# Kernel optimization log

Hardware: AMD Instinct MI355X
Metric: run time of the kernel (lower is better)

Reference implementation:

```python
import jax, jax.numpy as jnp
import numpy as np

C = 2000
P = 5_000_000
FX, FY, CX, CY = 1000.0, 1000.0, 320.0, 240.0


def setup_inputs() -> dict:
    key = jax.random.key(0)
    k1, k2, k3, k4, k5 = jax.random.split(key, 5)
    # SE3 poses: [tx,ty,tz, qx,qy,qz,qw] with unit quaternion (pypose randn_SE3 convention)
    t = jax.random.normal(k1, (C, 3), dtype=jnp.float32)
    q = jax.random.normal(k2, (C, 4), dtype=jnp.float32)
    q = q / jnp.linalg.norm(q, axis=-1, keepdims=True)
    poses = jnp.concatenate([t, q], axis=-1)  # [C,7]
    points_param = jax.random.normal(k3, (P, 3), dtype=jnp.float32)
    observes = jax.random.normal(k4, (P, 2), dtype=jnp.float32)
    K = jnp.array([[FX, 0.0, CX], [0.0, FY, CY], [0.0, 0.0, 1.0]], dtype=jnp.float32)
    cidx = jax.random.randint(k5, (P,), 0, C, dtype=jnp.int64)
    pidx = jnp.arange(P, dtype=jnp.int64)
    return {"poses": poses, "points_param": points_param, "observes": observes,
            "K": K, "cidx": cidx, "pidx": pidx}


def _se3_act(pose7, pts):
    # pose7: [P,7] = [t(3), q_xyz(3), q_w(1)]; pts: [P,3]
    t = pose7[:, 0:3]
    qv = pose7[:, 3:6]
    qw = pose7[:, 6:7]
    # rotated = p + 2*qv x (qv x p + qw*p)
    uv = jnp.cross(qv, pts) + qw * pts
    return pts + 2.0 * jnp.cross(qv, uv) + t


def reference(poses, points_param, observes, K, cidx, pidx):
    p = poses[cidx]            # [P,7] gather camera poses
    pts = points_param[pidx]   # [P,3] gather 3D points
    pc = _se3_act(p, pts)      # camera-frame points [P,3]
    proj = pc @ K.T            # [P,3] homogeneous pixels
    pix = proj[:, :2] / proj[:, 2:3]
    return pix - observes      # [P,2] residual
```

## Files before the change

### kernel.cpp

```cpp
#include <hip/hip_runtime.h>


__global__ __launch_bounds__(256) void residual_kernel(
    const float* __restrict__ poses,
    const float* __restrict__ pts,
    const float* __restrict__ obs,
    const float* __restrict__ Km,
    const int*   __restrict__ cidx,
    const int*   __restrict__ pidx,
    float*       __restrict__ out,
    int n4)
{
    int t = blockIdx.x * blockDim.x + threadIdx.x;
    if (t >= n4) return;

    float k00 = Km[0], k01 = Km[1], k02 = Km[2];
    float k10 = Km[3], k11 = Km[4], k12 = Km[5];
    float k20 = Km[6], k21 = Km[7], k22 = Km[8];

    int4 ci4 = ((const int4*)cidx)[t];
    int4 pi4 = ((const int4*)pidx)[t];
    float4 ob01 = ((const float4*)obs)[2 * t];
    float4 ob23 = ((const float4*)obs)[2 * t + 1];

    int cis[4]  = {ci4.x, ci4.y, ci4.z, ci4.w};
    int pis[4]  = {pi4.x, pi4.y, pi4.z, pi4.w};
    float ob[8] = {ob01.x, ob01.y, ob01.z, ob01.w, ob23.x, ob23.y, ob23.z, ob23.w};

    float res[8];

    #pragma unroll
    for (int j = 0; j < 4; ++j) {
        const float* pp = pts + 3L * (long)pis[j];
        float px = pp[0], py = pp[1], pz = pp[2];

        const float* po = poses + 7L * (long)cis[j];
        float tx = po[0], ty = po[1], tz = po[2];
        float qx = po[3], qy = po[4], qz = po[5], qw = po[6];

        float ux = qy * pz - qz * py + qw * px;
        float uy = qz * px - qx * pz + qw * py;
        float uz = qx * py - qy * px + qw * pz;

        float cx = px + 2.0f * (qy * uz - qz * uy) + tx;
        float cy = py + 2.0f * (qz * ux - qx * uz) + ty;
        float cz = pz + 2.0f * (qx * uy - qy * ux) + tz;

        float w    = k20 * cx + k21 * cy + k22 * cz;
        float invw = 1.0f / w;
        float u    = (k00 * cx + k01 * cy + k02 * cz) * invw;
        float v    = (k10 * cx + k11 * cy + k12 * cz) * invw;

        res[2 * j]     = u - ob[2 * j];
        res[2 * j + 1] = v - ob[2 * j + 1];
    }

    float4* o = (float4*)(out + 8L * (long)t);
    o[0] = make_float4(res[0], res[1], res[2], res[3]);
    o[1] = make_float4(res[4], res[5], res[6], res[7]);
}

extern "C" void kernel_launch(void* const* d_in, const int* in_sizes, int n_in,
                              void* d_out, int out_size, void* d_ws, size_t ws_size,
                              hipStream_t stream) {
    const float* poses = (const float*)d_in[0];
    const float* pts   = (const float*)d_in[1];
    const float* obs   = (const float*)d_in[2];
    const float* Km    = (const float*)d_in[3];
    const int*   cidx  = (const int*)d_in[4];
    const int*   pidx  = (const int*)d_in[5];
    float* out = (float*)d_out;

    int P  = in_sizes[4];
    int n4 = P / 4;

    const int block = 256;
    int grid = (n4 + block - 1) / block;
    residual_kernel<<<grid, block, 0, stream>>>(poses, pts, obs, Km, cidx, pidx, out, n4);
}
```

Baseline: 197.9 us.

## Stage camera poses in LDS and switch to persistent grid-stride kernel

Each block copies all C poses into shared memory, packed as two float4 slots per camera with a parity swizzle, and then serves per-observation pose reads from LDS instead of scattered global loads. The launch becomes a fixed 512x1024 persistent grid with a grid-stride loop so the staging cost is paid once per block. In exchange, every block performs a serial preload of 64KB of LDS data with strided global reads, and the large LDS footprint limits occupancy. The pose table was small and probably already L2-resident, so the benefit depends on how much the global gathers were actually costing.

Result: slower. 202.5 us (+2.3%).

```diff
diff --git a/kernel.cpp b/kernel.cpp
--- a/kernel.cpp
+++ b/kernel.cpp
@@ -1,7 +1,10 @@
 #include <hip/hip_runtime.h>
 
 
-__global__ __launch_bounds__(256) void residual_kernel(
+#define BLOCK 1024
+#define GRID  512
+
+__global__ __launch_bounds__(BLOCK) void residual_kernel(
     const float* __restrict__ poses,
     const float* __restrict__ pts,
     const float* __restrict__ obs,
@@ -9,55 +12,76 @@
     const int*   __restrict__ cidx,
     const int*   __restrict__ pidx,
     float*       __restrict__ out,
-    int n4)
+    int n4,
+    int C)
 {
-    int t = blockIdx.x * blockDim.x + threadIdx.x;
-    if (t >= n4) return;
+    extern __shared__ float spose[];
+
+    int tid = threadIdx.x;
+    int total = C * 7;
+    for (int idx = tid; idx < total; idx += BLOCK) {
+        int j = idx / 7;
+        int k = idx - j * 7;
+        int par  = j & 1;
+        int slot = (k < 4) ? (2 * j + par) : (2 * j + 1 - par);
+        int off  = (k < 4) ? k : (k - 4);
+        spose[slot * 4 + off] = poses[idx];
+    }
+    __syncthreads();
+
+    const float4* sp = (const float4*)spose;
 
     float k00 = Km[0], k01 = Km[1], k02 = Km[2];
     float k10 = Km[3], k11 = Km[4], k12 = Km[5];
     float k20 = Km[6], k21 = Km[7], k22 = Km[8];
 
-    int4 ci4 = ((const int4*)cidx)[t];
-    int4 pi4 = ((const int4*)pidx)[t];
-    float4 ob01 = ((const float4*)obs)[2 * t];
-    float4 ob23 = ((const float4*)obs)[2 * t + 1];
+    int stride = GRID * BLOCK;
+    for (int t = blockIdx.x * BLOCK + tid; t < n4; t += stride) {
+        int4 ci4 = ((const int4*)cidx)[t];
+        int4 pi4 = ((const int4*)pidx)[t];
+        float4 ob01 = ((const float4*)obs)[2 * t];
+        float4 ob23 = ((const float4*)obs)[2 * t + 1];
 
-    int cis[4]  = {ci4.x, ci4.y, ci4.z, ci4.w};
-    int pis[4]  = {pi4.x, pi4.y, pi4.z, pi4.w};
-    float ob[8] = {ob01.x, ob01.y, ob01.z, ob01.w, ob23.x, ob23.y, ob23.z, ob23.w};
+        int cis[4]  = {ci4.x, ci4.y, ci4.z, ci4.w};
+        int pis[4]  = {pi4.x, pi4.y, pi4.z, pi4.w};
+        float ob[8] = {ob01.x, ob01.y, ob01.z, ob01.w,
+                       ob23.x, ob23.y, ob23.z, ob23.w};
 
-    float res[8];
+        float res[8];
 
-    #pragma unroll
-    for (int j = 0; j < 4; ++j) {
-        const float* pp = pts + 3L * (long)pis[j];
-        float px = pp[0], py = pp[1], pz = pp[2];
+        #pragma unroll
+        for (int j = 0; j < 4; ++j) {
+            const float* pp = pts + 3L * (long)pis[j];
+            float px = pp[0], py = pp[1], pz = pp[2];
 
-        const float* po = poses + 7L * (long)cis[j];
-        float tx = po[0], ty = po[1], tz = po[2];
-        float qx = po[3], qy = po[4], qz = po[5], qw = po[6];
+            int ci  = cis[j];
+            int par = ci & 1;
+            float4 lo = sp[2 * ci + par];
+            float4 hi = sp[2 * ci + 1 - par];
+            float tx = lo.x, ty = lo.y, tz = lo.z;
+            float qx = lo.w, qy = hi.x, qz = hi.y, qw = hi.z;
 
-        float ux = qy * pz - qz * py + qw * px;
-        float uy = qz * px - qx * pz + qw * py;
-        float uz = qx * py - qy * px + qw * pz;
+            float ux = qy * pz - qz * py + qw * px;
+            float uy = qz * px - qx * pz + qw * py;
+            float uz = qx * py - qy * px + qw * pz;
 
-        float cx = px + 2.0f * (qy * uz - qz * uy) + tx;
-        float cy = py + 2.0f * (qz * ux - qx * uz) + ty;
-        float cz = pz + 2.0f * (qx * uy - qy * ux) + tz;
+            float cx = px + 2.0f * (qy * uz - qz * uy) + tx;
+            float cy = py + 2.0f * (qz * ux - qx * uz) + ty;
+            float cz = pz + 2.0f * (qx * uy - qy * ux) + tz;
 
-        float w    = k20 * cx + k21 * cy + k22 * cz;
-        float invw = 1.0f / w;
-        float u    = (k00 * cx + k01 * cy + k02 * cz) * invw;
-        float v    = (k10 * cx + k11 * cy + k12 * cz) * invw;
+            float w    = k20 * cx + k21 * cy + k22 * cz;
+            float invw = 1.0f / w;
+            float u    = (k00 * cx + k01 * cy + k02 * cz) * invw;
+            float v    = (k10 * cx + k11 * cy + k12 * cz) * invw;
 
-        res[2 * j]     = u - ob[2 * j];
-        res[2 * j + 1] = v - ob[2 * j + 1];
+            res[2 * j]     = u - ob[2 * j];
+            res[2 * j + 1] = v - ob[2 * j + 1];
+        }
+
+        float4* o = (float4*)(out + 8L * (long)t);
+        o[0] = make_float4(res[0], res[1], res[2], res[3]);
+        o[1] = make_float4(res[4], res[5], res[6], res[7]);
     }
-
-    float4* o = (float4*)(out + 8L * (long)t);
-    o[0] = make_float4(res[0], res[1], res[2], res[3]);
-    o[1] = make_float4(res[4], res[5], res[6], res[7]);
 }
 
 extern "C" void kernel_launch(void* const* d_in, const int* in_sizes, int n_in,
@@ -73,8 +97,9 @@
 
     int P  = in_sizes[4];
     int n4 = P / 4;
+    int C  = in_sizes[0] / 7;
 
-    const int block = 256;
-    int grid = (n4 + block - 1) / block;
-    residual_kernel<<<grid, block, 0, stream>>>(poses, pts, obs, Km, cidx, pidx, out, n4);
+    size_t lds_bytes = (size_t)C * 8 * sizeof(float);
+    residual_kernel<<<GRID, BLOCK, lds_bytes, stream>>>(
+        poses, pts, obs, Km, cidx, pidx, out, n4, C);
 }
```

## Pad pose table to float4 pairs, process 8 points per thread, use rcp

Applied to the files above, without the earlier changes.

Adds a small pre-kernel that repacks the 7-float poses into aligned pairs of float4 in workspace, so each camera gather becomes two vector loads. The main kernel now handles 8 points per thread, issuing all pose and point gathers before doing the math to raise memory-level parallelism. It also swaps the division for the hardware reciprocal. Costs include an extra launch, higher register pressure, and slightly lower-precision reciprocal.

New measurement: 212.1 us. +7.2%, slower.

```diff
diff --git a/kernel.cpp b/kernel.cpp
--- a/kernel.cpp
+++ b/kernel.cpp
@@ -1,63 +1,94 @@
 #include <hip/hip_runtime.h>
 
 
-__global__ __launch_bounds__(256) void residual_kernel(
-    const float* __restrict__ poses,
-    const float* __restrict__ pts,
-    const float* __restrict__ obs,
-    const float* __restrict__ Km,
-    const int*   __restrict__ cidx,
-    const int*   __restrict__ pidx,
-    float*       __restrict__ out,
-    int n4)
+#define BLOCK 256
+
+__global__ void pad_poses_kernel(const float* __restrict__ poses,
+                                 float4* __restrict__ ptab, int C) {
+    int j = blockIdx.x * blockDim.x + threadIdx.x;
+    if (j >= C) return;
+    const float* p = poses + 7L * j;
+    ptab[2 * j]     = make_float4(p[0], p[1], p[2], p[3]);
+    ptab[2 * j + 1] = make_float4(p[4], p[5], p[6], 0.0f);
+}
+
+__global__ __launch_bounds__(BLOCK) void residual_kernel(
+    const float4* __restrict__ ptab,
+    const float*  __restrict__ pts,
+    const float4* __restrict__ obs4,
+    const float*  __restrict__ Km,
+    const int4*   __restrict__ cidx4,
+    const int4*   __restrict__ pidx4,
+    float4*       __restrict__ out4,
+    int n8)
 {
-    int t = blockIdx.x * blockDim.x + threadIdx.x;
-    if (t >= n4) return;
+    int t = blockIdx.x * BLOCK + threadIdx.x;
+    if (t >= n8) return;
+
+    int4 ci_lo = cidx4[2 * t];
+    int4 ci_hi = cidx4[2 * t + 1];
+    int4 pi_lo = pidx4[2 * t];
+    int4 pi_hi = pidx4[2 * t + 1];
+    float4 ob[4];
+    #pragma unroll
+    for (int j = 0; j < 4; ++j) ob[j] = obs4[4 * t + j];
 
     float k00 = Km[0], k01 = Km[1], k02 = Km[2];
     float k10 = Km[3], k11 = Km[4], k12 = Km[5];
     float k20 = Km[6], k21 = Km[7], k22 = Km[8];
 
-    int4 ci4 = ((const int4*)cidx)[t];
-    int4 pi4 = ((const int4*)pidx)[t];
-    float4 ob01 = ((const float4*)obs)[2 * t];
-    float4 ob23 = ((const float4*)obs)[2 * t + 1];
+    int cis[8] = {ci_lo.x, ci_lo.y, ci_lo.z, ci_lo.w,
+                  ci_hi.x, ci_hi.y, ci_hi.z, ci_hi.w};
+    int pis[8] = {pi_lo.x, pi_lo.y, pi_lo.z, pi_lo.w,
+                  pi_hi.x, pi_hi.y, pi_hi.z, pi_hi.w};
 
-    int cis[4]  = {ci4.x, ci4.y, ci4.z, ci4.w};
-    int pis[4]  = {pi4.x, pi4.y, pi4.z, pi4.w};
-    float ob[8] = {ob01.x, ob01.y, ob01.z, ob01.w, ob23.x, ob23.y, ob23.z, ob23.w};
+    float4 plo[8], phi[8];
+    #pragma unroll
+    for (int j = 0; j < 8; ++j) {
+        plo[j] = ptab[2 * cis[j]];
+        phi[j] = ptab[2 * cis[j] + 1];
+    }
+    float px[8], py[8], pz[8];
+    #pragma unroll
+    for (int j = 0; j < 8; ++j) {
+        const float* pp = pts + 3L * (long)pis[j];
+        px[j] = pp[0]; py[j] = pp[1]; pz[j] = pp[2];
+    }
 
-    float res[8];
+    float res[16];
+    #pragma unroll
+    for (int j = 0; j < 8; ++j) {
+        float tx = plo[j].x, ty = plo[j].y, tz = plo[j].z;
+        float qx = plo[j].w, qy = phi[j].x, qz = phi[j].y, qw = phi[j].z;
+        float X = px[j], Y = py[j], Z = pz[j];
 
-    #pragma unroll
-    for (int j = 0; j < 4; ++j) {
-        const float* pp = pts + 3L * (long)pis[j];
-        float px = pp[0], py = pp[1], pz = pp[2];
+        float ux = qy * Z - qz * Y + qw * X;
+        float uy = qz * X - qx * Z + qw * Y;
+        float uz = qx * Y - qy * X + qw * Z;
 
-        const float* po = poses + 7L * (long)cis[j];
-        float tx = po[0], ty = po[1], tz = po[2];
-        float qx = po[3], qy = po[4], qz = po[5], qw = po[6];
-
-        float ux = qy * pz - qz * py + qw * px;
-        float uy = qz * px - qx * pz + qw * py;
-        float uz = qx * py - qy * px + qw * pz;
-
-        float cx = px + 2.0f * (qy * uz - qz * uy) + tx;
-        float cy = py + 2.0f * (qz * ux - qx * uz) + ty;
-        float cz = pz + 2.0f * (qx * uy - qy * ux) + tz;
+        float cx = X + 2.0f * (qy * uz - qz * uy) + tx;
+        float cy = Y + 2.0f * (qz * ux - qx * uz) + ty;
+        float cz = Z + 2.0f * (qx * uy - qy * ux) + tz;
 
         float w    = k20 * cx + k21 * cy + k22 * cz;
-        float invw = 1.0f / w;
+        float invw = __builtin_amdgcn_rcpf(w);
         float u    = (k00 * cx + k01 * cy + k02 * cz) * invw;
         float v    = (k10 * cx + k11 * cy + k12 * cz) * invw;
 
-        res[2 * j]     = u - ob[2 * j];
-        res[2 * j + 1] = v - ob[2 * j + 1];
+        float2 o  = make_float2(u, v);
+        res[2 * j]     = o.x;
+        res[2 * j + 1] = o.y;
     }
 
-    float4* o = (float4*)(out + 8L * (long)t);
-    o[0] = make_float4(res[0], res[1], res[2], res[3]);
-    o[1] = make_float4(res[4], res[5], res[6], res[7]);
+    res[0]  -= ob[0].x; res[1]  -= ob[0].y; res[2]  -= ob[0].z; res[3]  -= ob[0].w;
+    res[4]  -= ob[1].x; res[5]  -= ob[1].y; res[6]  -= ob[1].z; res[7]  -= ob[1].w;
+    res[8]  -= ob[2].x; res[9]  -= ob[2].y; res[10] -= ob[2].z; res[11] -= ob[2].w;
+    res[12] -= ob[3].x; res[13] -= ob[3].y; res[14] -= ob[3].z; res[15] -= ob[3].w;
+
+    #pragma unroll
+    for (int j = 0; j < 4; ++j)
+        out4[4 * t + j] = make_float4(res[4 * j], res[4 * j + 1],
+                                      res[4 * j + 2], res[4 * j + 3]);
 }
 
 extern "C" void kernel_launch(void* const* d_in, const int* in_sizes, int n_in,
@@ -72,9 +103,15 @@
     float* out = (float*)d_out;
 
     int P  = in_sizes[4];
-    int n4 = P / 4;
+    int C  = in_sizes[0] / 7;
+    int n8 = P / 8;
 
-    const int block = 256;
-    int grid = (n4 + block - 1) / block;
-    residual_kernel<<<grid, block, 0, stream>>>(poses, pts, obs, Km, cidx, pidx, out, n4);
+    float4* ptab = (float4*)d_ws;
+
+    pad_poses_kernel<<<(C + BLOCK - 1) / BLOCK, BLOCK, 0, stream>>>(poses, ptab, C);
+
+    int grid = (n8 + BLOCK - 1) / BLOCK;
+    residual_kernel<<<grid, BLOCK, 0, stream>>>(
+        ptab, pts, (const float4*)obs, Km,
+        (const int4*)cidx, (const int4*)pidx, (float4*)out, n8);
 }
```
